# Performance work log

Hardware: AMD Instinct MI355X
Metric: run time of the kernel (lower is better)

The kernel has to match this reference:

```python
import jax, jax.numpy as jnp
import numpy as np

R = 48          # n_comp (== n_comp_xy)
X = Y = Z = 300 # world_size
C = 27          # channels
N = 1_000_000   # query points
XYZ_MIN = 0.0
XYZ_MAX = 1.0


def _sample2d(plane, gh, gw):
    """Bilinear grid_sample, align_corners=True.
    plane: [R, H, W]; gh, gw: [N] normalized coords in [-1, 1] indexing H and W.
    Returns [N, R].
    """
    H, W = plane.shape[1], plane.shape[2]
    ih = (gh + 1.0) * 0.5 * (H - 1)
    iw = (gw + 1.0) * 0.5 * (W - 1)
    i0 = jnp.clip(jnp.floor(ih).astype(jnp.int32), 0, H - 1)
    j0 = jnp.clip(jnp.floor(iw).astype(jnp.int32), 0, W - 1)
    i1 = jnp.minimum(i0 + 1, H - 1)
    j1 = jnp.minimum(j0 + 1, W - 1)
    fh = (ih - i0.astype(ih.dtype))[:, None]  # [N,1]
    fw = (iw - j0.astype(iw.dtype))[:, None]
    p00 = plane[:, i0, j0].T  # [N,R]
    p01 = plane[:, i0, j1].T
    p10 = plane[:, i1, j0].T
    p11 = plane[:, i1, j1].T
    top = p00 * (1 - fw) + p01 * fw
    bot = p10 * (1 - fw) + p11 * fw
    return top * (1 - fh) + bot * fh


def _sample1d(vec, g):
    """Linear interp along length dim (width of the [*,*,L,1] torch vec is 1,
    sampled at 0 -> pure 1D interp).  vec: [R, L]; g: [N] in [-1,1] -> [N,R]."""
    L = vec.shape[1]
    ih = (g + 1.0) * 0.5 * (L - 1)
    i0 = jnp.clip(jnp.floor(ih).astype(jnp.int32), 0, L - 1)
    i1 = jnp.minimum(i0 + 1, L - 1)
    f = (ih - i0.astype(ih.dtype))[:, None]
    return vec[:, i0].T * (1 - f) + vec[:, i1].T * f


def setup_inputs() -> dict:
    key = jax.random.key(0)
    ks = jax.random.split(key, 8)
    return {
        "xyz": jax.random.uniform(ks[0], (N, 3), dtype=jnp.float32),
        "xy_plane": jax.random.normal(ks[1], (R, X, Y), dtype=jnp.float32) * 0.1,
        "xz_plane": jax.random.normal(ks[2], (R, X, Z), dtype=jnp.float32) * 0.1,
        "yz_plane": jax.random.normal(ks[3], (R, Y, Z), dtype=jnp.float32) * 0.1,
        "x_vec": jax.random.normal(ks[4], (R, X), dtype=jnp.float32) * 0.1,
        "y_vec": jax.random.normal(ks[5], (R, Y), dtype=jnp.float32) * 0.1,
        "z_vec": jax.random.normal(ks[6], (R, Z), dtype=jnp.float32) * 0.1,
        "f_vec": jax.random.uniform(ks[7], (3 * R, C), dtype=jnp.float32,
                                     minval=-0.1, maxval=0.1),
    }


def reference(xyz, xy_plane, xz_plane, yz_plane, x_vec, y_vec, z_vec, f_vec):
    # normalize to [-1, 1]
    g = (xyz - XYZ_MIN) / (XYZ_MAX - XYZ_MIN) * 2.0 - 1.0  # [N,3]
    gx, gy, gz = g[:, 0], g[:, 1], g[:, 2]
    xy_feat = _sample2d(xy_plane, gx, gy)  # [N,R]
    xz_feat = _sample2d(xz_plane, gx, gz)
    yz_feat = _sample2d(yz_plane, gy, gz)
    x_feat = _sample1d(x_vec, gx)
    y_feat = _sample1d(y_vec, gy)
    z_feat = _sample1d(z_vec, gz)
    feat = jnp.concatenate([xy_feat * z_feat, xz_feat * y_feat, yz_feat * x_feat],
                           axis=-1)  # [N, 3R]
    return feat @ f_vec  # [N, C]
```

## Files before the change

kernel.cpp:

```cpp
#include <hip/hip_runtime.h>

#define RR 48
#define GG 300
#define HW2 (GG * GG)
#define NPLANE (RR * HW2)
#define NVEC (RR * GG)
#define CC 27
#define NBUCK 32768
#define TP 64
#define FROW 148

#define TROWS 16
#define TCOLS 256
#define PCHUNK ((HW2 + TCOLS - 1) / TCOLS)
#define NPASS (RR / TROWS)
#define TPB3 (3 * NPASS * PCHUNK)
#define VBLK ((3 * NVEC + 255) / 256)
#define TROW2 260

struct Axis { int i0, i1; float f; };

__device__ __forceinline__ Axis axis_interp(float x) {
  float g = x * 2.0f - 1.0f;
  float ih = (g + 1.0f) * 0.5f * (float)(GG - 1);
  int i0 = (int)floorf(ih);
  i0 = i0 < 0 ? 0 : (i0 > GG - 1 ? GG - 1 : i0);
  int i1 = i0 + 1 > GG - 1 ? GG - 1 : i0 + 1;
  Axis a; a.i0 = i0; a.i1 = i1; a.f = ih - (float)i0;
  return a;
}

__device__ __forceinline__ unsigned part3(unsigned v) {
  unsigned r = 0;
  r |= (v & 1u);
  r |= (v & 2u) << 2;
  r |= (v & 4u) << 4;
  r |= (v & 8u) << 6;
  r |= (v & 16u) << 8;
  return r;
}

__device__ __forceinline__ int morton_key(float x, float y, float z) {
  int qx = (int)(x * 32.0f); qx = qx < 0 ? 0 : (qx > 31 ? 31 : qx);
  int qy = (int)(y * 32.0f); qy = qy < 0 ? 0 : (qy > 31 ? 31 : qy);
  int qz = (int)(z * 32.0f); qz = qz < 0 ? 0 : (qz > 31 ? 31 : qz);
  return (int)(part3((unsigned)qx) | (part3((unsigned)qy) << 1) | (part3((unsigned)qz) << 2));
}

__global__ void __launch_bounds__(256) hist_kernel(const float* __restrict__ xyz, int n,
                                                   int* __restrict__ offs) {
  int i = blockIdx.x * blockDim.x + threadIdx.x;
  if (i >= n) return;
  atomicAdd(&offs[morton_key(xyz[i * 3], xyz[i * 3 + 1], xyz[i * 3 + 2])], 1);
}

__global__ void __launch_bounds__(1024) scan_kernel(int* __restrict__ offs) {
  __shared__ int part[1024];
  int t = threadIdx.x;
  int base = t * (NBUCK / 1024);
  int loc[NBUCK / 1024];
  int s = 0;
#pragma unroll
  for (int i = 0; i < NBUCK / 1024; ++i) { loc[i] = offs[base + i]; s += loc[i]; }
  part[t] = s;
  __syncthreads();
  for (int off = 1; off < 1024; off <<= 1) {
    int u = (t >= off) ? part[t - off] : 0;
    __syncthreads();
    part[t] += u;
    __syncthreads();
  }
  int excl = (t == 0) ? 0 : part[t - 1];
#pragma unroll
  for (int i = 0; i < NBUCK / 1024; ++i) {
    int c = loc[i];
    offs[base + i] = excl;
    excl += c;
  }
}

__device__ __forceinline__ void plane_transpose_vb(
    int vb, int t, float* __restrict__ tile,
    const float* __restrict__ p0, const float* __restrict__ p1, const float* __restrict__ p2,
    float* __restrict__ t0, float* __restrict__ t1, float* __restrict__ t2) {
  int rem = vb;
  int plane = rem / (NPASS * PCHUNK);
  rem -= plane * (NPASS * PCHUNK);
  int pass = rem / PCHUNK;
  int chunk = rem - pass * PCHUNK;
  const float* in = (plane == 0) ? p0 : (plane == 1) ? p1 : p2;
  float* outp = (plane == 0) ? t0 : (plane == 1) ? t1 : t2;
  int base = chunk * TCOLS;
  int rbase = pass * TROWS;

  int p4 = t & 63;
  int rg = t >> 6;
#pragma unroll
  for (int i = 0; i < TROWS / 4; ++i) {
    int r = i * 4 + rg;
    int pos = base + p4 * 4;
    if (pos < HW2) {
      float4 v = *(const float4*)(in + (size_t)(rbase + r) * HW2 + pos);
      *(float4*)&tile[r * TROW2 + p4 * 4] = v;
    }
  }
  __syncthreads();

  int c4 = t & 3;
  int hwl = t >> 2;
#pragma unroll
  for (int jj = 0; jj < 4; ++jj) {
    int hw = jj * 64 + hwl;
    if (base + hw < HW2) {
      float4 w;
      w.x = tile[(c4 * 4 + 0) * TROW2 + hw];
      w.y = tile[(c4 * 4 + 1) * TROW2 + hw];
      w.z = tile[(c4 * 4 + 2) * TROW2 + hw];
      w.w = tile[(c4 * 4 + 3) * TROW2 + hw];
      *(float4*)(outp + (size_t)(base + hw) * RR + rbase + c4 * 4) = w;
    }
  }
}

__device__ __forceinline__ void vec_transpose_e(
    int e, const float* __restrict__ v0, const float* __restrict__ v1,
    const float* __restrict__ v2, float* __restrict__ tv0,
    float* __restrict__ tv1, float* __restrict__ tv2) {
  if (e < 3 * NVEC) {
    int v = e / NVEC;
    int rem = e - v * NVEC;
    int i = rem / RR;
    int r = rem - i * RR;
    const float* in = (v == 0) ? v0 : (v == 1) ? v1 : v2;
    float* out = (v == 0) ? tv0 : (v == 1) ? tv1 : tv2;
    out[i * RR + r] = in[r * GG + i];
  }
}

__global__ void __launch_bounds__(256) trans_scatter_kernel(
    const float* __restrict__ xyz, int n, int* __restrict__ offs,
    int* __restrict__ sidx, float4* __restrict__ sxyz, int scb,
    const float* __restrict__ p0, const float* __restrict__ p1, const float* __restrict__ p2,
    float* __restrict__ t0, float* __restrict__ t1, float* __restrict__ t2,
    const float* __restrict__ v0, const float* __restrict__ v1, const float* __restrict__ v2,
    float* __restrict__ tv0, float* __restrict__ tv1, float* __restrict__ tv2) {
  __shared__ float tile[TROWS * TROW2];
  int bb = blockIdx.x;
  int t = threadIdx.x;

  if (bb < scb) {
    int i = bb * 256 + t;
    if (i < n) {
      float x = xyz[i * 3], y = xyz[i * 3 + 1], z = xyz[i * 3 + 2];
      int key = morton_key(x, y, z);
      int pos = atomicAdd(&offs[key], 1);
      if (sxyz) sxyz[pos] = make_float4(x, y, z, __int_as_float(i));
      else      sidx[pos] = i;
    }
  } else if (bb < scb + TPB3) {
    plane_transpose_vb(bb - scb, t, tile, p0, p1, p2, t0, t1, t2);
  } else {
    vec_transpose_e((bb - scb - TPB3) * 256 + t, v0, v1, v2, tv0, tv1, tv2);
  }
}

__device__ __forceinline__ void gather_seg(const float* __restrict__ P, Axis ai, Axis aj,
                                           const float* __restrict__ V, Axis ak,
                                           int r4, float* __restrict__ dst) {
  float fi = ai.f, fj = aj.f, fk = ak.f;
  float w00 = (1.f - fi) * (1.f - fj);
  float w01 = (1.f - fi) * fj;
  float w10 = fi * (1.f - fj);
  float w11 = fi * fj;
  float omk = 1.f - fk;
  float4 q00 = *(const float4*)(P + (ai.i0 * GG + aj.i0) * RR + r4);
  float4 q01 = *(const float4*)(P + (ai.i0 * GG + aj.i1) * RR + r4);
  float4 q10 = *(const float4*)(P + (ai.i1 * GG + aj.i0) * RR + r4);
  float4 q11 = *(const float4*)(P + (ai.i1 * GG + aj.i1) * RR + r4);
  float4 b0 = *(const float4*)(V + ak.i0 * RR + r4);
  float4 b1 = *(const float4*)(V + ak.i1 * RR + r4);
  float4 o;
  o.x = (w00 * q00.x + w01 * q01.x + w10 * q10.x + w11 * q11.x) * (omk * b0.x + fk * b1.x);
  o.y = (w00 * q00.y + w01 * q01.y + w10 * q10.y + w11 * q11.y) * (omk * b0.y + fk * b1.y);
  o.z = (w00 * q00.z + w01 * q01.z + w10 * q10.z + w11 * q11.z) * (omk * b0.z + fk * b1.z);
  o.w = (w00 * q00.w + w01 * q01.w + w10 * q10.w + w11 * q11.w) * (omk * b0.w + fk * b1.w);
  *(float4*)(dst + r4) = o;
}

__global__ void __launch_bounds__(256, 4) tensorf_fused(
    const float4* __restrict__ sxyz, const int* __restrict__ sidx,
    const float* __restrict__ xyz,
    const float* __restrict__ Txy, const float* __restrict__ Txz, const float* __restrict__ Tyz,
    const float* __restrict__ Tx, const float* __restrict__ Ty, const float* __restrict__ Tz,
    const float* __restrict__ F, float* __restrict__ out, int n, int chunkLen) {
  __shared__ float featT[TP * FROW];
  __shared__ int oiS[TP];
  int b = blockIdx.x;
  int nb = (b & 7) * chunkLen + (b >> 3);
  int base = nb * TP;
  int tid = threadIdx.x;
  int g = tid >> 4;
  int l = tid & 15;

#pragma unroll 1
  for (int it = 0; it < TP / 16; ++it) {
    int pl = (it << 4) + g;
    int sp = base + pl;
    if (sp < n) {
      float x, y, z;
      int oi;
      if (sxyz) {
        float4 p4 = sxyz[sp];
        x = p4.x; y = p4.y; z = p4.z;
        oi = __float_as_int(p4.w);
      } else {
        oi = sidx[sp];
        x = xyz[oi * 3 + 0];
        y = xyz[oi * 3 + 1];
        z = xyz[oi * 3 + 2];
      }
      if (l == 12) oiS[pl] = oi;
      Axis ax = axis_interp(x), ay = axis_interp(y), az = axis_interp(z);
      if (l < 12) {
        int r4 = l << 2;
        float* dst = &featT[pl * FROW];
        gather_seg(Txy, ax, ay, Tz, az, r4, dst + 0 * RR);
        gather_seg(Txz, ax, az, Ty, ay, r4, dst + 1 * RR);
        gather_seg(Tyz, ay, az, Tx, ax, r4, dst + 2 * RR);
      }
    }
  }
  __syncthreads();

  int p = tid & (TP - 1);
  int q = __builtin_amdgcn_readfirstlane(tid >> 6);
  int cbase = (q == 3) ? 20 : q * 7;
  const float* Fh = F + cbase;
  const float* row = &featT[p * FROW];

  float acc[7];
#pragma unroll
  for (int c = 0; c < 7; ++c) acc[c] = 0.f;

#pragma unroll 4
  for (int k4 = 0; k4 < 36; ++k4) {
    float4 fv = *(const float4*)(row + 4 * k4);
    const float* Fr = Fh + (k4 * 4) * CC;
#pragma unroll
    for (int c = 0; c < 7; ++c) {
      acc[c] = fmaf(fv.w, Fr[3 * CC + c],
               fmaf(fv.z, Fr[2 * CC + c],
               fmaf(fv.y, Fr[CC + c],
               fmaf(fv.x, Fr[c], acc[c]))));
    }
  }

  int sp = base + p;
  if (sp < n) {
    int oi = oiS[p];
    float* o = out + (size_t)oi * CC + cbase;
    if (q != 3) o[0] = acc[0];
#pragma unroll
    for (int c = 1; c < 7; ++c) o[c] = acc[c];
  }
}

__global__ void __launch_bounds__(256) tensorf_naive(
    const float* __restrict__ xyz,
    const float* __restrict__ Pxy, const float* __restrict__ Pxz, const float* __restrict__ Pyz,
    const float* __restrict__ Vx, const float* __restrict__ Vy, const float* __restrict__ Vz,
    const float* __restrict__ F, float* __restrict__ out, int n) {
  int idx = blockIdx.x * blockDim.x + threadIdx.x;
  if (idx >= n) return;
  float x = xyz[idx * 3], y = xyz[idx * 3 + 1], z = xyz[idx * 3 + 2];
  Axis ax = axis_interp(x), ay = axis_interp(y), az = axis_interp(z);
  float acc[CC];
#pragma unroll
  for (int c = 0; c < CC; ++c) acc[c] = 0.f;
  const float* Ps[3] = {Pxy, Pxz, Pyz};
  const float* Vs[3] = {Vz, Vy, Vx};
  Axis A[3][2] = {{ax, ay}, {ax, az}, {ay, az}};
  Axis K[3] = {az, ay, ax};
#pragma unroll 1
  for (int s = 0; s < 3; ++s) {
    Axis ai = A[s][0], aj = A[s][1], ak = K[s];
    float fi = ai.f, fj = aj.f, fk = ak.f;
    float w00 = (1.f - fi) * (1.f - fj), w01 = (1.f - fi) * fj;
    float w10 = fi * (1.f - fj), w11 = fi * fj, omk = 1.f - fk;
#pragma unroll 1
    for (int r = 0; r < RR; ++r) {
      const float* pr = Ps[s] + r * HW2;
      float ft = (w00 * pr[ai.i0 * GG + aj.i0] + w01 * pr[ai.i0 * GG + aj.i1] +
                  w10 * pr[ai.i1 * GG + aj.i0] + w11 * pr[ai.i1 * GG + aj.i1]) *
                 (omk * Vs[s][r * GG + ak.i0] + fk * Vs[s][r * GG + ak.i1]);
      const float* Fr = F + (s * RR + r) * CC;
#pragma unroll
      for (int c = 0; c < CC; ++c) acc[c] = fmaf(ft, Fr[c], acc[c]);
    }
  }
  float* o = out + (size_t)idx * CC;
#pragma unroll
  for (int c = 0; c < CC; ++c) o[c] = acc[c];
}

extern "C" void kernel_launch(void* const* d_in, const int* in_sizes, int n_in,
                              void* d_out, int out_size, void* d_ws, size_t ws_size,
                              hipStream_t stream) {
  const float* xyz = (const float*)d_in[0];
  const float* pxy = (const float*)d_in[1];
  const float* pxz = (const float*)d_in[2];
  const float* pyz = (const float*)d_in[3];
  const float* vx = (const float*)d_in[4];
  const float* vy = (const float*)d_in[5];
  const float* vz = (const float*)d_in[6];
  const float* F = (const float*)d_in[7];
  float* out = (float*)d_out;
  int n = in_sizes[0] / 3;
  int nblk = (n + 255) / 256;

  size_t fixed = (size_t)(3 * NPLANE + 3 * NVEC) * sizeof(float) +
                 (size_t)NBUCK * sizeof(int);
  size_t need1 = fixed + (size_t)n * sizeof(int);
  size_t need2 = fixed + (size_t)n * sizeof(float4);

  if (ws_size >= need1) {
    float* w = (float*)d_ws;
    float* Txy = w;
    float* Txz = Txy + NPLANE;
    float* Tyz = Txz + NPLANE;
    float* Tx = Tyz + NPLANE;
    float* Ty = Tx + NVEC;
    float* Tz = Ty + NVEC;
    int* offs = (int*)(Tz + NVEC);

    int* sidx = nullptr;
    float4* sxyz = nullptr;
    if (ws_size >= need2) sxyz = (float4*)(offs + NBUCK);
    else sidx = (int*)(offs + NBUCK);

    hipMemsetAsync(offs, 0, (size_t)NBUCK * sizeof(int), stream);
    hist_kernel<<<nblk, 256, 0, stream>>>(xyz, n, offs);
    scan_kernel<<<1, 1024, 0, stream>>>(offs);
    trans_scatter_kernel<<<nblk + TPB3 + VBLK, 256, 0, stream>>>(
        xyz, n, offs, sidx, sxyz, nblk,
        pxy, pxz, pyz, Txy, Txz, Tyz, vx, vy, vz, Tx, Ty, Tz);

    int ntile = (n + TP - 1) / TP;
    int chunkLen = (ntile + 7) / 8;
    tensorf_fused<<<chunkLen * 8, 256, 0, stream>>>(sxyz, sidx, xyz, Txy, Txz, Tyz,
                                                    Tx, Ty, Tz, F, out, n, chunkLen);
  } else {
    tensorf_naive<<<nblk, 256, 0, stream>>>(xyz, pxy, pxz, pyz, vx, vy, vz, F, out, n);
  }
}
```

Measured before the change: 537.7 us.

## Drop Morton-order point sorting and gather points in input order

Removes the histogram, scan and scatter passes that bucketed query points by Morton key, along with the XCD-interleaved block remap. The fused kernel now reads xyz directly and writes output rows contiguously. This saves three launches, the atomics and the scatter traffic, but loses spatial locality in the plane gathers, which become random accesses over about 52 MB of transposed planes.

After: 514.0 us. 4.4% less time.

```diff
diff --git a/kernel.cpp b/kernel.cpp
--- a/kernel.cpp
+++ b/kernel.cpp
@@ -6,7 +6,6 @@
 #define NPLANE (RR * HW2)
 #define NVEC (RR * GG)
 #define CC 27
-#define NBUCK 32768
 #define TP 64
 #define FROW 148
 
@@ -28,55 +27,6 @@
   int i1 = i0 + 1 > GG - 1 ? GG - 1 : i0 + 1;
   Axis a; a.i0 = i0; a.i1 = i1; a.f = ih - (float)i0;
   return a;
-}
-
-__device__ __forceinline__ unsigned part3(unsigned v) {
-  unsigned r = 0;
-  r |= (v & 1u);
-  r |= (v & 2u) << 2;
-  r |= (v & 4u) << 4;
-  r |= (v & 8u) << 6;
-  r |= (v & 16u) << 8;
-  return r;
-}
-
-__device__ __forceinline__ int morton_key(float x, float y, float z) {
-  int qx = (int)(x * 32.0f); qx = qx < 0 ? 0 : (qx > 31 ? 31 : qx);
-  int qy = (int)(y * 32.0f); qy = qy < 0 ? 0 : (qy > 31 ? 31 : qy);
-  int qz = (int)(z * 32.0f); qz = qz < 0 ? 0 : (qz > 31 ? 31 : qz);
-  return (int)(part3((unsigned)qx) | (part3((unsigned)qy) << 1) | (part3((unsigned)qz) << 2));
-}
-
-__global__ void __launch_bounds__(256) hist_kernel(const float* __restrict__ xyz, int n,
-                                                   int* __restrict__ offs) {
-  int i = blockIdx.x * blockDim.x + threadIdx.x;
-  if (i >= n) return;
-  atomicAdd(&offs[morton_key(xyz[i * 3], xyz[i * 3 + 1], xyz[i * 3 + 2])], 1);
-}
-
-__global__ void __launch_bounds__(1024) scan_kernel(int* __restrict__ offs) {
-  __shared__ int part[1024];
-  int t = threadIdx.x;
-  int base = t * (NBUCK / 1024);
-  int loc[NBUCK / 1024];
-  int s = 0;
-#pragma unroll
-  for (int i = 0; i < NBUCK / 1024; ++i) { loc[i] = offs[base + i]; s += loc[i]; }
-  part[t] = s;
-  __syncthreads();
-  for (int off = 1; off < 1024; off <<= 1) {
-    int u = (t >= off) ? part[t - off] : 0;
-    __syncthreads();
-    part[t] += u;
-    __syncthreads();
-  }
-  int excl = (t == 0) ? 0 : part[t - 1];
-#pragma unroll
-  for (int i = 0; i < NBUCK / 1024; ++i) {
-    int c = loc[i];
-    offs[base + i] = excl;
-    excl += c;
-  }
 }
 
 __device__ __forceinline__ void plane_transpose_vb(
@@ -137,9 +87,7 @@
   }
 }
 
-__global__ void __launch_bounds__(256) trans_scatter_kernel(
-    const float* __restrict__ xyz, int n, int* __restrict__ offs,
-    int* __restrict__ sidx, float4* __restrict__ sxyz, int scb,
+__global__ void __launch_bounds__(256) transpose_kernel(
     const float* __restrict__ p0, const float* __restrict__ p1, const float* __restrict__ p2,
     float* __restrict__ t0, float* __restrict__ t1, float* __restrict__ t2,
     const float* __restrict__ v0, const float* __restrict__ v1, const float* __restrict__ v2,
@@ -147,20 +95,10 @@
   __shared__ float tile[TROWS * TROW2];
   int bb = blockIdx.x;
   int t = threadIdx.x;
-
-  if (bb < scb) {
-    int i = bb * 256 + t;
-    if (i < n) {
-      float x = xyz[i * 3], y = xyz[i * 3 + 1], z = xyz[i * 3 + 2];
-      int key = morton_key(x, y, z);
-      int pos = atomicAdd(&offs[key], 1);
-      if (sxyz) sxyz[pos] = make_float4(x, y, z, __int_as_float(i));
-      else      sidx[pos] = i;
-    }
-  } else if (bb < scb + TPB3) {
-    plane_transpose_vb(bb - scb, t, tile, p0, p1, p2, t0, t1, t2);
+  if (bb < TPB3) {
+    plane_transpose_vb(bb, t, tile, p0, p1, p2, t0, t1, t2);
   } else {
-    vec_transpose_e((bb - scb - TPB3) * 256 + t, v0, v1, v2, tv0, tv1, tv2);
+    vec_transpose_e((bb - TPB3) * 256 + t, v0, v1, v2, tv0, tv1, tv2);
   }
 }
 
@@ -188,16 +126,12 @@
 }
 
 __global__ void __launch_bounds__(256, 4) tensorf_fused(
-    const float4* __restrict__ sxyz, const int* __restrict__ sidx,
     const float* __restrict__ xyz,
     const float* __restrict__ Txy, const float* __restrict__ Txz, const float* __restrict__ Tyz,
     const float* __restrict__ Tx, const float* __restrict__ Ty, const float* __restrict__ Tz,
-    const float* __restrict__ F, float* __restrict__ out, int n, int chunkLen) {
+    const float* __restrict__ F, float* __restrict__ out, int n) {
   __shared__ float featT[TP * FROW];
-  __shared__ int oiS[TP];
-  int b = blockIdx.x;
-  int nb = (b & 7) * chunkLen + (b >> 3);
-  int base = nb * TP;
+  int base = blockIdx.x * TP;
   int tid = threadIdx.x;
   int g = tid >> 4;
   int l = tid & 15;
@@ -207,19 +141,9 @@
     int pl = (it << 4) + g;
     int sp = base + pl;
     if (sp < n) {
-      float x, y, z;
-      int oi;
-      if (sxyz) {
-        float4 p4 = sxyz[sp];
-        x = p4.x; y = p4.y; z = p4.z;
-        oi = __float_as_int(p4.w);
-      } else {
-        oi = sidx[sp];
-        x = xyz[oi * 3 + 0];
-        y = xyz[oi * 3 + 1];
-        z = xyz[oi * 3 + 2];
-      }
-      if (l == 12) oiS[pl] = oi;
+      float x = xyz[sp * 3 + 0];
+      float y = xyz[sp * 3 + 1];
+      float z = xyz[sp * 3 + 2];
       Axis ax = axis_interp(x), ay = axis_interp(y), az = axis_interp(z);
       if (l < 12) {
         int r4 = l << 2;
@@ -257,8 +181,7 @@
 
   int sp = base + p;
   if (sp < n) {
-    int oi = oiS[p];
-    float* o = out + (size_t)oi * CC + cbase;
+    float* o = out + (size_t)sp * CC + cbase;
     if (q != 3) o[0] = acc[0];
 #pragma unroll
     for (int c = 1; c < 7; ++c) o[c] = acc[c];
@@ -318,12 +241,9 @@
   int n = in_sizes[0] / 3;
   int nblk = (n + 255) / 256;
 
-  size_t fixed = (size_t)(3 * NPLANE + 3 * NVEC) * sizeof(float) +
-                 (size_t)NBUCK * sizeof(int);
-  size_t need1 = fixed + (size_t)n * sizeof(int);
-  size_t need2 = fixed + (size_t)n * sizeof(float4);
-
-  if (ws_size >= need1) {
+  size_t need = (size_t)(3 * NPLANE + 3 * NVEC) * sizeof(float);
+
+  if (ws_size >= need) {
     float* w = (float*)d_ws;
     float* Txy = w;
     float* Txz = Txy + NPLANE;
@@ -331,24 +251,13 @@
     float* Tx = Tyz + NPLANE;
     float* Ty = Tx + NVEC;
     float* Tz = Ty + NVEC;
-    int* offs = (int*)(Tz + NVEC);
-
-    int* sidx = nullptr;
-    float4* sxyz = nullptr;
-    if (ws_size >= need2) sxyz = (float4*)(offs + NBUCK);
-    else sidx = (int*)(offs + NBUCK);
-
-    hipMemsetAsync(offs, 0, (size_t)NBUCK * sizeof(int), stream);
-    hist_kernel<<<nblk, 256, 0, stream>>>(xyz, n, offs);
-    scan_kernel<<<1, 1024, 0, stream>>>(offs);
-    trans_scatter_kernel<<<nblk + TPB3 + VBLK, 256, 0, stream>>>(
-        xyz, n, offs, sidx, sxyz, nblk,
+
+    transpose_kernel<<<TPB3 + VBLK, 256, 0, stream>>>(
         pxy, pxz, pyz, Txy, Txz, Tyz, vx, vy, vz, Tx, Ty, Tz);
 
     int ntile = (n + TP - 1) / TP;
-    int chunkLen = (ntile + 7) / 8;
-    tensorf_fused<<<chunkLen * 8, 256, 0, stream>>>(sxyz, sidx, xyz, Txy, Txz, Tyz,
-                                                    Tx, Ty, Tz, F, out, n, chunkLen);
+    tensorf_fused<<<ntile, 256, 0, stream>>>(xyz, Txy, Txz, Tyz,
+                                             Tx, Ty, Tz, F, out, n);
   } else {
     tensorf_naive<<<nblk, 256, 0, stream>>>(xyz, pxy, pxz, pyz, vx, vy, vz, F, out, n);
   }
```
